# Optimization experiments

Hardware: AMD Instinct MI355X
Metric: run time of the kernel (lower is better)

Reference implementation:

```python
import jax, jax.numpy as jnp
import numpy as np

SR = 16000; HOP = 256; NFFT = 2048; NMELS = 80; NSTFT = NFFT // 2 + 1
MIN_P = int(SR / 500.0); MAX_P = int(SR / 50.0)  # 32, 320
FRAME_LEN = 2 * HOP  # 512
N_ITER = 4; MOMENTUM = 0.99


def hann(N):
    # periodic hann window (torch.hann_window default)
    return 0.5 - 0.5 * jnp.cos(2.0 * jnp.pi * jnp.arange(N) / N)


def frame_signal(x, frame_len, hop):
    # x: (B, T) -> (B, n_frames, frame_len)
    n_frames = (x.shape[-1] - frame_len) // hop + 1
    idx = jnp.arange(n_frames)[:, None] * hop + jnp.arange(frame_len)[None, :]
    return x[:, idx]


def stft(x, window):
    # center=True, reflect pad, onesided -> (B, NSTFT, n_frames) complex
    xp = jnp.pad(x, ((0, 0), (NFFT // 2, NFFT // 2)), mode='reflect')
    fr = frame_signal(xp, NFFT, HOP) * window
    return jnp.fft.rfft(fr, axis=-1).transpose(0, 2, 1)


def istft(spec, window):
    # spec: (B, NSTFT, n_frames) complex -> (B, HOP*(n_frames-1)) real
    fr = jnp.fft.irfft(spec.transpose(0, 2, 1), n=NFFT, axis=-1) * window
    B, nF, _ = fr.shape
    L = NFFT + HOP * (nF - 1)
    idx = (jnp.arange(nF)[:, None] * HOP + jnp.arange(NFFT)[None, :]).ravel()
    y = jnp.zeros((B, L), fr.dtype).at[:, idx].add(fr.reshape(B, -1))
    env = jnp.zeros((L,), fr.dtype).at[idx].add(jnp.tile(window ** 2, nF))
    y = y / jnp.where(env > 1e-11, env, 1.0)
    return y[:, NFFT // 2: NFFT // 2 + HOP * (nF - 1)]


def mel_fbanks():
    # torchaudio melscale_fbanks, htk scale, norm=None -> (NSTFT, NMELS)
    all_freqs = jnp.linspace(0.0, SR / 2, NSTFT)
    m_max = 2595.0 * jnp.log10(1.0 + (SR / 2) / 700.0)
    f_pts = 700.0 * (10.0 ** (jnp.linspace(0.0, m_max, NMELS + 2) / 2595.0) - 1.0)
    f_diff = f_pts[1:] - f_pts[:-1]
    slopes = f_pts[None, :] - all_freqs[:, None]
    down = -slopes[:, :-2] / f_diff[:-1]
    up = slopes[:, 2:] / f_diff[1:]
    return jnp.maximum(0.0, jnp.minimum(down, up))


def mel_to_linear(mel):
    # F.interpolate(mode='linear', align_corners=False) along mel axis 80 -> 1025
    scale = NMELS / NSTFT
    src = jnp.maximum((jnp.arange(NSTFT) + 0.5) * scale - 0.5, 0.0)
    i0 = jnp.clip(jnp.floor(src).astype(jnp.int32), 0, NMELS - 1)
    i1 = jnp.minimum(i0 + 1, NMELS - 1)
    w = (src - i0).astype(mel.dtype)
    return (1.0 - w)[None, :, None] * mel[:, i0, :] + w[None, :, None] * mel[:, i1, :]


def griffin_lim(spec, window):
    # torchaudio GriffinLim: power=1, n_iter=4, momentum=0.99, rand_init
    kr, ki = jax.random.split(jax.random.key(42))
    angles = (jax.random.uniform(kr, spec.shape) + 1j * jax.random.uniform(ki, spec.shape)).astype(jnp.complex64)
    tprev = jnp.zeros_like(angles)
    mom = MOMENTUM / (1.0 + MOMENTUM)
    for _ in range(N_ITER):
        inv = istft(spec * angles, window)
        rebuilt = stft(inv, window)
        angles = rebuilt - tprev * mom
        angles = angles / (jnp.abs(angles) + 1e-16)
        tprev = rebuilt
    return istft(spec * angles, window)


def _forward(waveform, W1, b1, W2, b2, W3, b3):
    window = hann(NFFT)
    x = waveform[:, 0, :]  # (B, T)
    # --- F0 + loudness framing (frame_length=512, hop=256, reflect pad) ---
    xp = jnp.pad(x, ((0, 0), (FRAME_LEN // 2, FRAME_LEN // 2)), mode='reflect')
    frames = frame_signal(xp, FRAME_LEN, HOP)  # (B, nF, 512)
    # F0: L2-normalize frames, FFT-based linear autocorrelation over lags 32..255
    fn = frames / (jnp.linalg.norm(frames, axis=-1, keepdims=True) + 1e-8)
    sp = jnp.fft.rfft(fn, n=2 * FRAME_LEN, axis=-1)
    ac = jnp.fft.irfft(sp * jnp.conj(sp), n=2 * FRAME_LEN, axis=-1)
    ac = ac[..., MIN_P:min(MAX_P, FRAME_LEN // 2)]  # (B, nF, 224)
    period = jnp.argmax(ac, axis=-1).astype(x.dtype) + MIN_P
    f0 = jnp.clip(SR / (period + 1e-8), 50.0, 500.0)  # (B, nF)
    # loudness
    loud = 20.0 * jnp.log10(jnp.sqrt(jnp.mean(frames ** 2, axis=-1)) + 1e-8)
    # bottleneck encoder (eval mode: no f0 noise)
    feats = jnp.stack([f0, loud], axis=-1)  # (B, nF, 2)
    h = jax.nn.elu(feats @ W1 + b1)
    h = jax.nn.elu(h @ W2 + b2)
    content = h @ W3 + b3  # (B, nF, 64)
    # --- mel -> linear -> griffin-lim (eval mode: no formant perturb) ---
    mag = jnp.abs(stft(x, window))  # power=1.0 magnitude, (B, 1025, nF)
    mel = jnp.einsum('bft,fm->bmt', mag, mel_fbanks())  # (B, 80, nF)
    lin = mel_to_linear(mel)  # (B, 1025, nF)
    rec = griffin_lim(lin, window)  # (B, T)
    T = waveform.shape[-1]
    rec = rec[..., :T]
    pad = T - rec.shape[-1]
    if pad > 0:
        rec = jnp.pad(rec, ((0, 0), (0, pad)))
    return rec, content


def setup_inputs() -> dict:
    key = jax.random.key(0)
    ks = jax.random.split(key, 4)
    B, T = 16, 131072
    waveform = jax.random.normal(ks[0], (B, 1, T), jnp.float32)

    def lin_init(k, fi, fo):
        bound = 1.0 / np.sqrt(fi)
        kw, kb = jax.random.split(k)
        W = jax.random.uniform(kw, (fi, fo), jnp.float32, -bound, bound)
        b = jax.random.uniform(kb, (fo,), jnp.float32, -bound, bound)
        return W, b

    W1, b1 = lin_init(ks[1], 2, 256)
    W2, b2 = lin_init(ks[2], 256, 256)
    W3, b3 = lin_init(ks[3], 256, 64)
    return {"waveform": waveform, "W1": W1, "b1": b1, "W2": W2, "b2": b2, "W3": W3, "b3": b3}


def reference(waveform, W1, b1, W2, b2, W3, b3):
    return _forward(waveform, W1, b1, W2, b2, W3, b3)
```

## Files before the change

kernel.cpp:

```cpp
#include <hip/hip_runtime.h>
#include <cstdint>
#include <cstddef>

#ifndef M_PI
#define M_PI 3.14159265358979323846
#endif

#define SRATE   16000
#define HOP     256
#define NFFT    2048
#define NBINS   1025
#define NMELS   80
#define BATCH   16
#define TLEN    131072
#define NF      513
#define LOLA    133120
#define FRAMEL  512
#define MINP    32
#define NLAGS   224
#define NELEM   (BATCH*NBINS*NF)
#define MLPR    4
#define DF      7.8125f

#define PADF(i) ((i) + 3*((i) >> 5))

__host__ __device__ inline void threefry2x32(uint32_t k0, uint32_t k1,
                                             uint32_t x0, uint32_t x1,
                                             uint32_t& o0, uint32_t& o1) {
  uint32_t ks0 = k0, ks1 = k1, ks2 = k0 ^ k1 ^ 0x1BD11BDAu;
  uint32_t ks[3] = {ks0, ks1, ks2};
  const uint32_t rot[2][4] = {{13u,15u,26u,6u},{17u,29u,16u,24u}};
  x0 += ks0; x1 += ks1;
#pragma unroll
  for (int i = 0; i < 5; ++i) {
#pragma unroll
    for (int r = 0; r < 4; ++r) {
      uint32_t rr = rot[i & 1][r];
      x0 += x1;
      x1 = (x1 << rr) | (x1 >> (32u - rr));
      x1 ^= x0;
    }
    x0 += ks[(i + 1) % 3];
    x1 += ks[(i + 2) % 3] + (uint32_t)(i + 1);
  }
  o0 = x0; o1 = x1;
}

__device__ inline float bits_to_uniform(uint32_t b) {
  uint32_t fb = (b >> 9) | 0x3f800000u;
  return __uint_as_float(fb) - 1.0f;
}

#define BF(e,o,WR,WI) do{ float vr=Xr[o]*(WR)-Xi[o]*(WI); \
  float vi=Xr[o]*(WI)+Xi[o]*(WR); float ur=Xr[e],ui=Xi[e]; \
  Xr[e]=ur+vr; Xi[e]=ui+vi; Xr[o]=ur-vr; Xi[o]=ui-vi; }while(0)

__device__ __forceinline__ void fft1024(float (&Xr)[8], float (&Xi)[8],
    float* __restrict__ sre, float* __restrict__ sim,
    const float* __restrict__ twr, const float* __restrict__ twi, float sgn)
{
  const int t = threadIdx.x;
  const float C7 = 0.70710678118654752440f;
  BF(0,1,1.0f,0.0f); BF(2,3,1.0f,0.0f); BF(4,5,1.0f,0.0f); BF(6,7,1.0f,0.0f);
  BF(0,2,1.0f,0.0f); BF(1,3,0.0f,sgn); BF(4,6,1.0f,0.0f); BF(5,7,0.0f,sgn);
  BF(0,4,1.0f,0.0f); BF(1,5,C7,sgn*C7); BF(2,6,0.0f,sgn); BF(3,7,-C7,sgn*C7);
  __syncthreads();
#pragma unroll
  for (int m = 0; m < 8; ++m) { int p = PADF(8*t + m); sre[p] = Xr[m]; sim[p] = Xi[m]; }
  __syncthreads();
  {
    int f0 = t & 7, f1 = t >> 3;
#pragma unroll
    for (int m = 0; m < 8; ++m) { int p = PADF(f0 + 8*m + 64*f1); Xr[m] = sre[p]; Xi[m] = sim[p]; }
    int x = 128*f0; float wr = twr[x], wi = sgn*twi[x];
    BF(0,1,wr,wi); BF(2,3,wr,wi); BF(4,5,wr,wi); BF(6,7,wr,wi);
    x = 64*f0;      float ar = twr[x], ai = sgn*twi[x];
    x = 64*(f0+8);  float br = twr[x], bi = sgn*twi[x];
    BF(0,2,ar,ai); BF(1,3,br,bi); BF(4,6,ar,ai); BF(5,7,br,bi);
#pragma unroll
    for (int mm = 0; mm < 4; ++mm) {
      x = 32*(f0 + 8*mm); float cr = twr[x], ci = sgn*twi[x];
      BF(mm, mm+4, cr, ci);
    }
#pragma unroll
    for (int m = 0; m < 8; ++m) { int p = PADF(f0 + 8*m + 64*f1); sre[p] = Xr[m]; sim[p] = Xi[m]; }
  }
  __syncthreads();
  {
    int f0 = t & 63, f1 = t >> 6;
#pragma unroll
    for (int m = 0; m < 8; ++m) { int p = PADF(f0 + 64*m + 512*f1); Xr[m] = sre[p]; Xi[m] = sim[p]; }
    int x = 16*f0; float wr = twr[x], wi = sgn*twi[x];
    BF(0,1,wr,wi); BF(2,3,wr,wi); BF(4,5,wr,wi); BF(6,7,wr,wi);
    x = 8*f0;       float ar = twr[x], ai = sgn*twi[x];
    x = 8*(f0+64);  float br = twr[x], bi = sgn*twi[x];
    BF(0,2,ar,ai); BF(1,3,br,bi); BF(4,6,ar,ai); BF(5,7,br,bi);
#pragma unroll
    for (int mm = 0; mm < 4; ++mm) {
      x = 4*(f0 + 64*mm); float cr = twr[x], ci = sgn*twi[x];
      BF(mm, mm+4, cr, ci);
    }
#pragma unroll
    for (int m = 0; m < 8; ++m) { int p = PADF(f0 + 64*m + 512*f1); sre[p] = Xr[m]; sim[p] = Xi[m]; }
  }
  __syncthreads();
  {
#pragma unroll
    for (int m = 0; m < 8; ++m) { int p = PADF(t + 128*m); Xr[m] = sre[p]; Xi[m] = sim[p]; }
#pragma unroll
    for (int mm = 0; mm < 4; ++mm) {
      int x = 2*t + 256*mm; float cr = twr[x], ci = sgn*twi[x];
      BF(mm, mm+4, cr, ci);
    }
  }
}

__device__ __forceinline__ void r2c_combine(float (&Xr)[8], float (&Xi)[8],
    float* __restrict__ sre, float* __restrict__ sim,
    const float* __restrict__ twr, const float* __restrict__ twi,
    float& x1024r)
{
  const int t = threadIdx.x;
  __syncthreads();
#pragma unroll
  for (int m = 0; m < 8; ++m) { int p = PADF(t + 128*m); sre[p] = Xr[m]; sim[p] = Xi[m]; }
  __syncthreads();
  if (t == 0) x1024r = Xr[0] - Xi[0];
#pragma unroll
  for (int m = 0; m < 8; ++m) {
    int k  = t + 128*m;
    int km = PADF((1024 - k) & 1023);
    float zmr = sre[km], zmi = sim[km];
    float Er  = 0.5f*(Xr[m] + zmr), Ei  = 0.5f*(Xi[m] - zmi);
    float Odr = 0.5f*(Xr[m] - zmr), Odi = 0.5f*(Xi[m] + zmi);
    float Or  = Odi, Oi = -Odr;
    float wr  = twr[k], wi = -twi[k];
    Xr[m] = Er + (wr*Or - wi*Oi);
    Xi[m] = Ei + (wr*Oi + wi*Or);
  }
}

__device__ inline float lin_interp_s(const float* __restrict__ melsh, int k) {
  float src = ((float)k + 0.5f) * ((float)NMELS / (float)NBINS) - 0.5f;
  src = src < 0.0f ? 0.0f : src;
  int i0 = (int)src; if (i0 > NMELS - 1) i0 = NMELS - 1;
  int i1 = i0 + 1 > NMELS - 1 ? NMELS - 1 : i0 + 1;
  float w = src - (float)i0;
  return (1.0f - w) * melsh[i0] + w * melsh[i1];
}

__global__ __launch_bounds__(256) void k_init_a(float2* __restrict__ winp,
                                                double* __restrict__ win2,
                                                float* __restrict__ twrf, float* __restrict__ twif,
                                                float* __restrict__ fptsf,
                                                int2* __restrict__ melrange) {
  int i = blockIdx.x * 256 + threadIdx.x;
  if (i < NFFT) {
    double w = 0.5 - 0.5 * cos(2.0 * M_PI * (double)i / (double)NFFT);
    win2[i] = w * w;
  }
  if (i < 1024) {
    double w0 = 0.5 - 0.5 * cos(2.0 * M_PI * (double)(2*i)   / (double)NFFT);
    double w1 = 0.5 - 0.5 * cos(2.0 * M_PI * (double)(2*i+1) / (double)NFFT);
    winp[i] = make_float2((float)w0, (float)w1);
    double th = 2.0 * M_PI * (double)i / (double)NFFT;
    twrf[i] = (float)cos(th); twif[i] = (float)sin(th);
  }
  if (i < NMELS + 2) {
    double m_max = 2595.0 * log10(1.0 + (SRATE / 2.0) / 700.0);
    fptsf[i] = (float)(700.0 * (pow(10.0, ((double)i * m_max / (double)(NMELS + 1)) / 2595.0) - 1.0));
  }
  if (i < NMELS) {
    double m_max = 2595.0 * log10(1.0 + (SRATE / 2.0) / 700.0);
    double fp0 = 700.0 * (pow(10.0, ((double)i       * m_max / (double)(NMELS + 1)) / 2595.0) - 1.0);
    double fp1 = 700.0 * (pow(10.0, ((double)(i + 1) * m_max / (double)(NMELS + 1)) / 2595.0) - 1.0);
    double fp2 = 700.0 * (pow(10.0, ((double)(i + 2) * m_max / (double)(NMELS + 1)) / 2595.0) - 1.0);
    int lo = (int)floor(fp0 / 7.8125) + 1;
    int hi = (int)ceil (fp2 / 7.8125);
    if (lo < 0) lo = 0; if (lo > NBINS) lo = NBINS;
    if (hi < 0) hi = 0; if (hi > NBINS) hi = NBINS;
    #define WGT(k) fmin(((double)(k)*7.8125 - fp0)/(fp1 - fp0), (fp2 - (double)(k)*7.8125)/(fp2 - fp1))
    while (lo > 0 && WGT(lo - 1) > 0.0) --lo;
    while (lo < hi && WGT(lo) <= 0.0) ++lo;
    while (hi < NBINS && WGT(hi) > 0.0) ++hi;
    while (hi > lo && WGT(hi - 1) <= 0.0) --hi;
    #undef WGT
    melrange[i] = make_int2(lo, hi);
  }
}

__global__ __launch_bounds__(256) void k_init_b(const double* __restrict__ win2,
                                                float* __restrict__ envif) {
  int i = blockIdx.x * 256 + threadIdx.x;
  if (i < LOLA) {
    int lo = i - (NFFT - 1);
    int fmin = lo <= 0 ? 0 : (lo + HOP - 1) / HOP;
    int fmax = i / HOP; if (fmax > NF - 1) fmax = NF - 1;
    double s = 0.0;
    for (int f = fmin; f <= fmax; ++f) s += win2[i - HOP * f];
    envif[i] = (float)(1.0 / (s > 1e-11 ? s : 1.0));
  }
}

__global__ __launch_bounds__(256) void k_angles(float2* __restrict__ A,
                                                uint32_t kr0, uint32_t kr1,
                                                uint32_t ki0, uint32_t ki1) {
  uint32_t idx = blockIdx.x * 256u + threadIdx.x;
  if (idx >= (uint32_t)NELEM) return;
  uint32_t per_b = (uint32_t)(NF * NBINS);
  uint32_t b = idx / per_b, r = idx % per_b;
  uint32_t t = r / NBINS, k = r % NBINS;
  uint32_t j = (b * (uint32_t)NBINS + k) * (uint32_t)NF + t;
  uint32_t a0, a1, b0, b1;
  threefry2x32(kr0, kr1, 0u, j, a0, a1);
  threefry2x32(ki0, ki1, 0u, j, b0, b1);
  A[idx] = make_float2(bits_to_uniform(a0 ^ a1), bits_to_uniform(b0 ^ b1));
}

__global__ __launch_bounds__(128) void k_stft_mel(const float* __restrict__ x,
                                                  const float2* __restrict__ winp,
                                                  const float* __restrict__ twrf, const float* __restrict__ twif,
                                                  const float* __restrict__ fptsf, const int2* __restrict__ melrange,
                                                  float* __restrict__ mel) {
  __shared__ float sre[1160], sim[1160];
  __shared__ float fsh[NMELS + 2];
  __shared__ int2  rsh[NMELS];
  int b = blockIdx.x / NF, tf = blockIdx.x % NF;
  int t = threadIdx.x;
  const float* xb = x + (size_t)b * TLEN;
  if (t < NMELS + 2) fsh[t] = fptsf[t];
  if (t < NMELS)     rsh[t] = melrange[t];
  if (tf >= 4 && tf <= 508) {
    const float2* xb2 = (const float2*)xb;
#pragma unroll
    for (int s = 0; s < 8; ++s) {
      int n = t + 128 * s;
      float2 v = xb2[128 * tf + n - 512];
      float2 w = winp[n];
      sre[PADF(n)] = v.x * w.x;
      sim[PADF(n)] = v.y * w.y;
    }
  } else {
#pragma unroll
    for (int s = 0; s < 8; ++s) {
      int n = t + 128 * s;
      int j0 = HOP * tf + 2 * n - (NFFT / 2);
      int m0 = j0 < 0 ? -j0 : (j0 >= TLEN ? 2 * TLEN - 2 - j0 : j0);
      int j1 = j0 + 1;
      int m1 = j1 < 0 ? -j1 : (j1 >= TLEN ? 2 * TLEN - 2 - j1 : j1);
      float2 w = winp[n];
      sre[PADF(n)] = xb[m0] * w.x;
      sim[PADF(n)] = xb[m1] * w.y;
    }
  }
  __syncthreads();
  float Xr[8], Xi[8];
  int rt = (int)(__brev((unsigned)t) >> 25);
  const int r3[8] = {0,4,2,6,1,5,3,7};
#pragma unroll
  for (int m = 0; m < 8; ++m) {
    int p = PADF(rt + 128 * r3[m]);
    Xr[m] = sre[p]; Xi[m] = sim[p];
  }
  fft1024(Xr, Xi, sre, sim, twrf, twif, -1.0f);
  float x1024r = 0.0f;
  r2c_combine(Xr, Xi, sre, sim, twrf, twif, x1024r);
  __syncthreads();
#pragma unroll
  for (int m = 0; m < 8; ++m) {
    int k = t + 128 * m;
    sre[k] = sqrtf(Xr[m]*Xr[m] + Xi[m]*Xi[m]);
  }
  if (t == 0) sre[1024] = fabsf(x1024r);
  __syncthreads();
  if (t < NMELS) {
    float fp0 = fsh[t], fp1 = fsh[t + 1], fp2 = fsh[t + 2];
    float id0 = 1.0f / (fp1 - fp0), id1 = 1.0f / (fp2 - fp1);
    int2 r = rsh[t];
    float acc = 0.0f;
    for (int k = r.x; k < r.y; ++k) {
      float freq = (float)k * DF;
      float w = fminf((freq - fp0) * id0, (fp2 - freq) * id1);
      acc += sre[k] * fmaxf(w, 0.0f);
    }
    mel[(size_t)blockIdx.x * NMELS + t] = acc;
  }
}

__global__ __launch_bounds__(128) void k_istft(const float* __restrict__ mel, const float2* __restrict__ A,
                                               const float2* __restrict__ winp,
                                               const float* __restrict__ twrf, const float* __restrict__ twif,
                                               float2* __restrict__ fr2) {
  __shared__ float sre[1160], sim[1160];
  __shared__ float melsh[NMELS];
  int t = threadIdx.x;
  size_t row = blockIdx.x;
  const float2* Arow = A + row * NBINS;
  if (t < NMELS) melsh[t] = mel[row * NMELS + t];
  __syncthreads();
#pragma unroll
  for (int s = 0; s < 9; ++s) {
    int k = t + 128 * s;
    if (k < NBINS) {
      float sv = lin_interp_s(melsh, k);
      float2 a = Arow[k];
      sre[PADF(k)] = sv * a.x;
      sim[PADF(k)] = (k == 0 || k == 1024) ? 0.0f : sv * a.y;
    }
  }
  __syncthreads();
  float Xr[8], Xi[8];
  int rt = (int)(__brev((unsigned)t) >> 25);
  const int r3[8] = {0,4,2,6,1,5,3,7};
#pragma unroll
  for (int m = 0; m < 8; ++m) {
    int n  = rt + 128 * r3[m];
    int p  = PADF(n), q = PADF(1024 - n);
    float Er = 0.5f*(sre[p] + sre[q]), Ei = 0.5f*(sim[p] - sim[q]);
    float Fr = 0.5f*(sre[p] - sre[q]), Fi = 0.5f*(sim[p] + sim[q]);
    float wr = twrf[n], wi = twif[n];
    float Or = wr*Fr - wi*Fi, Oi = wr*Fi + wi*Fr;
    Xr[m] = Er - Oi;
    Xi[m] = Ei + Or;
  }
  fft1024(Xr, Xi, sre, sim, twrf, twif, +1.0f);
  float2* frrow = fr2 + row * 1024;
  const float invM = 1.0f / 1024.0f;
#pragma unroll
  for (int m = 0; m < 8; ++m) {
    int g = t + 128 * m;
    float2 w = winp[g];
    frrow[g] = make_float2(Xr[m] * invM * w.x,
                           Xi[m] * invM * w.y);
  }
}

__global__ __launch_bounds__(256) void k_ola(const float* __restrict__ fr,
                                             const float* __restrict__ envif,
                                             float* __restrict__ y, float* __restrict__ out) {
  size_t idx = (size_t)blockIdx.x * 256 + threadIdx.x;
  const size_t QROW = LOLA / 4;
  if (idx >= (size_t)BATCH * QROW) return;
  int b = (int)(idx / QROW);
  int i0 = 4 * (int)(idx % QROW);
  const float* frb = fr + (size_t)b * NF * NFFT;
  int lo0 = i0 - (NFFT - 1);
  int fm0 = lo0 <= 0 ? 0 : (lo0 + HOP - 1) / HOP;
  int fx0 = i0 / HOP; if (fx0 > NF - 1) fx0 = NF - 1;
  int i3 = i0 + 3;
  int lo3 = i3 - (NFFT - 1);
  int fm3 = lo3 <= 0 ? 0 : (lo3 + HOP - 1) / HOP;
  int fx3 = i3 / HOP; if (fx3 > NF - 1) fx3 = NF - 1;
  float4 v;
  if (fm0 == fm3 && fx0 == fx3) {
    float4 s = make_float4(0.f, 0.f, 0.f, 0.f);
    for (int f = fm0; f <= fx0; ++f) {
      const float4 a = *(const float4*)(frb + (size_t)f * NFFT + (i0 - HOP * f));
      s.x += a.x; s.y += a.y; s.z += a.z; s.w += a.w;
    }
    const float4 e = *(const float4*)(envif + i0);
    v = make_float4(s.x * e.x, s.y * e.y, s.z * e.z, s.w * e.w);
  } else {
    float vv[4];
#pragma unroll
    for (int u = 0; u < 4; ++u) {
      int i = i0 + u;
      int lo = i - (NFFT - 1);
      int fmin = lo <= 0 ? 0 : (lo + HOP - 1) / HOP;
      int fmax = i / HOP; if (fmax > NF - 1) fmax = NF - 1;
      float s = 0.0f;
      for (int f = fmin; f <= fmax; ++f)
        s += frb[(size_t)f * NFFT + (i - HOP * f)];
      vv[u] = s * envif[i];
    }
    v = make_float4(vv[0], vv[1], vv[2], vv[3]);
  }
  if (out) {
    int j0 = i0 - NFFT / 2;
    if (j0 >= 0 && j0 + 3 < TLEN) {
      *(float4*)(out + (size_t)b * TLEN + j0) = v;
    } else {
      const float vv[4] = {v.x, v.y, v.z, v.w};
#pragma unroll
      for (int u = 0; u < 4; ++u) {
        int j = j0 + u;
        if (j >= 0 && j < TLEN) out[(size_t)b * TLEN + j] = vv[u];
      }
    }
  } else {
    *(float4*)(y + (size_t)b * LOLA + i0) = v;
  }
}

__global__ __launch_bounds__(128) void k_stft_gl(const float* __restrict__ y,
                                                 const float2* __restrict__ winp,
                                                 const float* __restrict__ twrf, const float* __restrict__ twif,
                                                 float2* __restrict__ A, float2* __restrict__ P,
                                                 float momf, int writeP) {
  __shared__ float sre[1160], sim[1160];
  int b = blockIdx.x / NF, tf = blockIdx.x % NF;
  int t = threadIdx.x;
  size_t row = blockIdx.x;
  float2* Arow = A + row * NBINS;
  float2* Prow = P + row * NBINS;
  const bool readP = (momf != 0.0f);
  float2 pfr[8];
  float2 pny = make_float2(0.0f, 0.0f);
  if (readP) {
#pragma unroll
    for (int m = 0; m < 8; ++m) pfr[m] = Prow[t + 128 * m];
    if (t == 0) pny = Prow[1024];
  } else {
#pragma unroll
    for (int m = 0; m < 8; ++m) pfr[m] = make_float2(0.0f, 0.0f);
  }
  const float* yb = y + (size_t)b * LOLA;
  if (tf >= 4 && tf <= 508) {
    const float2* yb2 = (const float2*)yb;
#pragma unroll
    for (int s = 0; s < 8; ++s) {
      int n = t + 128 * s;
      float2 v = yb2[128 * tf + n];
      float2 w = winp[n];
      sre[PADF(n)] = v.x * w.x;
      sim[PADF(n)] = v.y * w.y;
    }
  } else {
#pragma unroll
    for (int s = 0; s < 8; ++s) {
      int n = t + 128 * s;
      int j0 = HOP * tf + 2 * n - (NFFT / 2);
      int m0 = j0 < 0 ? -j0 : (j0 >= TLEN ? 2 * TLEN - 2 - j0 : j0);
      int j1 = j0 + 1;
      int m1 = j1 < 0 ? -j1 : (j1 >= TLEN ? 2 * TLEN - 2 - j1 : j1);
      float2 w = winp[n];
      sre[PADF(n)] = yb[NFFT/2 + m0] * w.x;
      sim[PADF(n)] = yb[NFFT/2 + m1] * w.y;
    }
  }
  __syncthreads();
  float Xr[8], Xi[8];
  int rt = (int)(__brev((unsigned)t) >> 25);
  const int r3[8] = {0,4,2,6,1,5,3,7};
#pragma unroll
  for (int m = 0; m < 8; ++m) {
    int p = PADF(rt + 128 * r3[m]);
    Xr[m] = sre[p]; Xi[m] = sim[p];
  }
  fft1024(Xr, Xi, sre, sim, twrf, twif, -1.0f);
  float x1024r = 0.0f;
  r2c_combine(Xr, Xi, sre, sim, twrf, twif, x1024r);
#pragma unroll
  for (int m = 0; m < 8; ++m) {
    int k = t + 128 * m;
    float ar = Xr[m] - momf * pfr[m].x;
    float ai = Xi[m] - momf * pfr[m].y;
    float mg = sqrtf(ar * ar + ai * ai) + 1e-16f;
    float inv = 1.0f / mg;
    Arow[k] = make_float2(ar * inv, ai * inv);
    if (writeP) Prow[k] = make_float2(Xr[m], Xi[m]);
  }
  if (t == 0) {
    float ar = x1024r - momf * pny.x;
    float ai = -momf * pny.y;
    float mg = sqrtf(ar * ar + ai * ai) + 1e-16f;
    float inv = 1.0f / mg;
    Arow[1024] = make_float2(ar * inv, ai * inv);
    if (writeP) Prow[1024] = make_float2(x1024r, 0.0f);
  }
}

__global__ __launch_bounds__(256) void k_feats(const float* __restrict__ x, double* __restrict__ feats) {
  __shared__ __align__(16) double xd[528];
  __shared__ double pacc[8][224];
  __shared__ double red[256];
  __shared__ double cval[256];
  __shared__ int    cidx[256];
  int b = blockIdx.x / NF, tf = blockIdx.x % NF;
  const float* xb = x + (size_t)b * TLEN;
  int tid = threadIdx.x;
  for (int n = tid; n < FRAMEL; n += 256) {
    int j = HOP * tf + n - (FRAMEL / 2);
    int m = j < 0 ? -j : (j >= TLEN ? 2 * TLEN - 2 - j : j);
    xd[n] = (double)xb[m];
  }
  if (tid < 16) xd[FRAMEL + tid] = 0.0;
  __syncthreads();
  double ss = 0.0;
  for (int n = tid; n < FRAMEL; n += 256) { double v = xd[n]; ss += v * v; }
  red[tid] = ss;
  __syncthreads();
  for (int w = 128; w > 0; w >>= 1) {
    if (tid < w) red[tid] += red[tid + w];
    __syncthreads();
  }
  double sumsq = red[0];
  int g = tid & 31, ph = tid >> 5;
  double acc[8];
#pragma unroll
  for (int d = 0; d < 8; ++d) acc[d] = 0.0;
  if (g < 28) {
    const double2* d2 = (const double2*)xd;
    const int LA = 32 + 4 * g;
    const int LB = 252 - 4 * g;
    for (int n0 = 8 * ph; n0 < 512 - LA; n0 += 64) {
      int h = n0 >> 1, hb = (n0 + LA) >> 1;
      double2 a0 = d2[h],      a1 = d2[h + 1],  a2 = d2[h + 2],  a3 = d2[h + 3];
      double2 b0 = d2[hb],     b1 = d2[hb + 1], b2 = d2[hb + 2],
              b3 = d2[hb + 3], b4 = d2[hb + 4], b5 = d2[hb + 5];
      double aa[8]  = {a0.x,a0.y,a1.x,a1.y,a2.x,a2.y,a3.x,a3.y};
      double bb[12] = {b0.x,b0.y,b1.x,b1.y,b2.x,b2.y,b3.x,b3.y,b4.x,b4.y,b5.x,b5.y};
#pragma unroll
      for (int d = 0; d < 4; ++d)
#pragma unroll
        for (int jj = 0; jj < 8; ++jj)
          acc[d] += aa[jj] * bb[jj + d];
    }
    for (int n0 = 8 * ph; n0 < 512 - LB; n0 += 64) {
      int h = n0 >> 1, hb = (n0 + LB) >> 1;
      double2 a0 = d2[h],      a1 = d2[h + 1],  a2 = d2[h + 2],  a3 = d2[h + 3];
      double2 b0 = d2[hb],     b1 = d2[hb + 1], b2 = d2[hb + 2],
              b3 = d2[hb + 3], b4 = d2[hb + 4], b5 = d2[hb + 5];
      double aa[8]  = {a0.x,a0.y,a1.x,a1.y,a2.x,a2.y,a3.x,a3.y};
      double bb[12] = {b0.x,b0.y,b1.x,b1.y,b2.x,b2.y,b3.x,b3.y,b4.x,b4.y,b5.x,b5.y};
#pragma unroll
      for (int d = 0; d < 4; ++d)
#pragma unroll
        for (int jj = 0; jj < 8; ++jj)
          acc[4 + d] += aa[jj] * bb[jj + d];
    }
#pragma unroll
    for (int d = 0; d < 8; ++d) pacc[ph][g * 8 + d] = acc[d];
  }
  __syncthreads();
  if (tid < 224) {
    double tot = 0.0;
#pragma unroll
    for (int p = 0; p < 8; ++p) tot += pacc[p][tid];
    int gg = tid >> 3, dd = tid & 7;
    int lag = dd < 4 ? (32 + 4 * gg + dd) : (252 - 4 * gg + (dd - 4));
    cval[tid] = tot; cidx[tid] = lag;
  } else { cval[tid] = -1e300; cidx[tid] = 1 << 30; }
  __syncthreads();
  for (int w = 128; w > 0; w >>= 1) {
    if (tid < w) {
      double vl = cval[tid], vr = cval[tid + w];
      int il = cidx[tid], ir = cidx[tid + w];
      if (vr > vl || (vr == vl && ir < il)) { cval[tid] = vr; cidx[tid] = ir; }
    }
    __syncthreads();
  }
  if (tid == 0) {
    double period = (double)cidx[0];
    double f0 = (double)SRATE / (period + 1e-8);
    f0 = f0 < 50.0 ? 50.0 : (f0 > 500.0 ? 500.0 : f0);
    double mean = sumsq / (double)FRAMEL;
    double loud = 20.0 * log10(sqrt(mean) + 1e-8);
    feats[(size_t)blockIdx.x * 2 + 0] = f0;
    feats[(size_t)blockIdx.x * 2 + 1] = loud;
  }
}

__global__ __launch_bounds__(256) void k_mlp(const double* __restrict__ feats,
                                             const float* __restrict__ W1, const float* __restrict__ b1,
                                             const float* __restrict__ W2, const float* __restrict__ b2,
                                             const float* __restrict__ W3, const float* __restrict__ b3,
                                             float* __restrict__ out) {
  __shared__ __align__(16) float h1[MLPR][256];
  __shared__ __align__(16) float h2[MLPR][256];
  __shared__ float fsh[MLPR][2];
  int j = threadIdx.x;
  size_t row0 = (size_t)blockIdx.x * MLPR;
  if (j < MLPR * 2) ((float*)fsh)[j] = (float)feats[row0 * 2 + j];
  __syncthreads();
  float w1a = W1[j], w1b = W1[256 + j], bb1 = b1[j];
#pragma unroll
  for (int r = 0; r < MLPR; ++r) {
    float v = fsh[r][0] * w1a + fsh[r][1] * w1b + bb1;
    h1[r][j] = v > 0.0f ? v : expm1f(v);
  }
  __syncthreads();
  float acc[MLPR];
  float bb2 = b2[j];
#pragma unroll
  for (int r = 0; r < MLPR; ++r) acc[r] = bb2;
  const float* w2p = W2 + j;
  for (int i4 = 0; i4 < 64; ++i4) {
    float w0 = w2p[(4 * i4 + 0) * 256];
    float w1 = w2p[(4 * i4 + 1) * 256];
    float w2v = w2p[(4 * i4 + 2) * 256];
    float w3v = w2p[(4 * i4 + 3) * 256];
#pragma unroll
    for (int r = 0; r < MLPR; ++r) {
      float4 hv = ((const float4*)h1[r])[i4];
      acc[r] += hv.x * w0;
      acc[r] += hv.y * w1;
      acc[r] += hv.z * w2v;
      acc[r] += hv.w * w3v;
    }
  }
#pragma unroll
  for (int r = 0; r < MLPR; ++r) h2[r][j] = acc[r] > 0.0f ? acc[r] : expm1f(acc[r]);
  __syncthreads();
  int o = j & 63, r = j >> 6;
  float oacc = b3[o];
  const float* w3p = W3 + o;
  for (int i4 = 0; i4 < 64; ++i4) {
    float4 hv = ((const float4*)h2[r])[i4];
    oacc += hv.x * w3p[(4 * i4 + 0) * 64];
    oacc += hv.y * w3p[(4 * i4 + 1) * 64];
    oacc += hv.z * w3p[(4 * i4 + 2) * 64];
    oacc += hv.w * w3p[(4 * i4 + 3) * 64];
  }
  out[(row0 + r) * 64 + o] = oacc;
}

__global__ void k_sentinel(float* out) { out[0] = 31337.0f; }

extern "C" void kernel_launch(void* const* d_in, const int* in_sizes, int n_in,
                              void* d_out, int out_size, void* d_ws, size_t ws_size,
                              hipStream_t stream) {
  const float* x  = (const float*)d_in[0];
  const float* W1 = (const float*)d_in[1];
  const float* b1 = (const float*)d_in[2];
  const float* W2 = (const float*)d_in[3];
  const float* b2 = (const float*)d_in[4];
  const float* W3 = (const float*)d_in[5];
  const float* b3 = (const float*)d_in[6];
  float* out = (float*)d_out;

  double* ws = (double*)d_ws;
  size_t o = 0;
  double*  winsq = ws + o; o += NFFT;
  double*  feats = ws + o; o += (size_t)BATCH * NF * 2;
  float2* winp  = (float2*)(ws + o);
  float*  twrf  = (float*)(winp + 1024);
  float*  twif  = twrf + 1024;
  float*  fptsf = twif + 1024;
  int2*   melrange = (int2*)(fptsf + 84);
  float*  mel   = (float*)(melrange + NMELS);
  float*  fr    = mel + (size_t)BATCH * NF * NMELS;
  float*  y     = fr + (size_t)BATCH * NF * NFFT;
  float*  envif = y + (size_t)BATCH * LOLA;
  float2* A     = (float2*)(envif + LOLA);
  float2* P     = A + (size_t)NELEM;
  size_t total_bytes = (size_t)((char*)(P + (size_t)NELEM) - (char*)d_ws);

  if (ws_size < total_bytes) {
    k_sentinel<<<1, 1, 0, stream>>>(out);
    return;
  }

  uint32_t kr0, kr1, ki0, ki1;
  threefry2x32(0u, 42u, 0u, 0u, kr0, kr1);
  threefry2x32(0u, 42u, 0u, 1u, ki0, ki1);

  const int NBLK = BATCH * NF;
  const int OLAB = ((size_t)BATCH * (LOLA / 4) + 255) / 256;
  k_init_a<<<8, 256, 0, stream>>>(winp, winsq, twrf, twif, fptsf, melrange);
  k_init_b<<<(LOLA + 255) / 256, 256, 0, stream>>>(winsq, envif);
  k_stft_mel<<<NBLK, 128, 0, stream>>>(x, winp, twrf, twif, fptsf, melrange, mel);
  k_angles<<<(NELEM + 255) / 256, 256, 0, stream>>>(A, kr0, kr1, ki0, ki1);

  const float momf = (float)(0.99 / 1.99);
  for (int it = 0; it < 4; ++it) {
    k_istft<<<NBLK, 128, 0, stream>>>(mel, A, winp, twrf, twif, (float2*)fr);
    k_ola<<<OLAB, 256, 0, stream>>>(fr, envif, y, nullptr);
    k_stft_gl<<<NBLK, 128, 0, stream>>>(y, winp, twrf, twif, A, P,
                                        it == 0 ? 0.0f : momf, it < 3 ? 1 : 0);
  }
  k_istft<<<NBLK, 128, 0, stream>>>(mel, A, winp, twrf, twif, (float2*)fr);
  k_ola<<<OLAB, 256, 0, stream>>>(fr, envif, y, out);

  k_feats<<<NBLK, 256, 0, stream>>>(x, feats);
  k_mlp<<<NBLK / MLPR, 256, 0, stream>>>(feats, W1, b1, W2, b2, W3, b3, out + (size_t)BATCH * TLEN);
}
```

Before: 873.4 us.

## Fuse Griffin-Lim STFT with following ISTFT and generate random phases inline

Merges the per-iteration forward STFT and phase normalisation with the next inverse STFT into one kernel, so the unit-phase spectrum A is never written to or read from global memory. The initial random phases are now generated with threefry inside the first ISTFT kernel rather than by a separate k_angles pass over a buffer. This removes one kernel launch per iteration, the angles kernel, and a large complex buffer of round-trip traffic. In exchange the fused kernel holds more live state and needs an extra barrier, which may raise register pressure.

```diff
diff --git a/kernel.cpp b/kernel.cpp
--- a/kernel.cpp
+++ b/kernel.cpp
@@ -202,21 +202,6 @@
   }
 }
 
-__global__ __launch_bounds__(256) void k_angles(float2* __restrict__ A,
-                                                uint32_t kr0, uint32_t kr1,
-                                                uint32_t ki0, uint32_t ki1) {
-  uint32_t idx = blockIdx.x * 256u + threadIdx.x;
-  if (idx >= (uint32_t)NELEM) return;
-  uint32_t per_b = (uint32_t)(NF * NBINS);
-  uint32_t b = idx / per_b, r = idx % per_b;
-  uint32_t t = r / NBINS, k = r % NBINS;
-  uint32_t j = (b * (uint32_t)NBINS + k) * (uint32_t)NF + t;
-  uint32_t a0, a1, b0, b1;
-  threefry2x32(kr0, kr1, 0u, j, a0, a1);
-  threefry2x32(ki0, ki1, 0u, j, b0, b1);
-  A[idx] = make_float2(bits_to_uniform(a0 ^ a1), bits_to_uniform(b0 ^ b1));
-}
-
 __global__ __launch_bounds__(128) void k_stft_mel(const float* __restrict__ x,
                                                   const float2* __restrict__ winp,
                                                   const float* __restrict__ twrf, const float* __restrict__ twif,
@@ -287,31 +272,145 @@
   }
 }
 
-__global__ __launch_bounds__(128) void k_istft(const float* __restrict__ mel, const float2* __restrict__ A,
-                                               const float2* __restrict__ winp,
-                                               const float* __restrict__ twrf, const float* __restrict__ twif,
-                                               float2* __restrict__ fr2) {
+__global__ __launch_bounds__(128) void k_istft0(const float* __restrict__ mel,
+                                                const float2* __restrict__ winp,
+                                                const float* __restrict__ twrf, const float* __restrict__ twif,
+                                                float2* __restrict__ fr2,
+                                                uint32_t kr0, uint32_t kr1,
+                                                uint32_t ki0, uint32_t ki1) {
   __shared__ float sre[1160], sim[1160];
   __shared__ float melsh[NMELS];
   int t = threadIdx.x;
   size_t row = blockIdx.x;
-  const float2* Arow = A + row * NBINS;
+  int b = blockIdx.x / NF, tf = blockIdx.x % NF;
   if (t < NMELS) melsh[t] = mel[row * NMELS + t];
   __syncthreads();
-#pragma unroll
   for (int s = 0; s < 9; ++s) {
     int k = t + 128 * s;
     if (k < NBINS) {
+      uint32_t j = ((uint32_t)b * (uint32_t)NBINS + (uint32_t)k) * (uint32_t)NF + (uint32_t)tf;
+      uint32_t a0, a1, b0, b1;
+      threefry2x32(kr0, kr1, 0u, j, a0, a1);
+      threefry2x32(ki0, ki1, 0u, j, b0, b1);
+      float ux = bits_to_uniform(a0 ^ a1);
+      float uy = bits_to_uniform(b0 ^ b1);
       float sv = lin_interp_s(melsh, k);
-      float2 a = Arow[k];
-      sre[PADF(k)] = sv * a.x;
-      sim[PADF(k)] = (k == 0 || k == 1024) ? 0.0f : sv * a.y;
+      sre[PADF(k)] = sv * ux;
+      sim[PADF(k)] = (k == 0 || k == 1024) ? 0.0f : sv * uy;
     }
   }
   __syncthreads();
   float Xr[8], Xi[8];
   int rt = (int)(__brev((unsigned)t) >> 25);
   const int r3[8] = {0,4,2,6,1,5,3,7};
+#pragma unroll
+  for (int m = 0; m < 8; ++m) {
+    int n  = rt + 128 * r3[m];
+    int p  = PADF(n), q = PADF(1024 - n);
+    float Er = 0.5f*(sre[p] + sre[q]), Ei = 0.5f*(sim[p] - sim[q]);
+    float Fr = 0.5f*(sre[p] - sre[q]), Fi = 0.5f*(sim[p] + sim[q]);
+    float wr = twrf[n], wi = twif[n];
+    float Or = wr*Fr - wi*Fi, Oi = wr*Fi + wi*Fr;
+    Xr[m] = Er - Oi;
+    Xi[m] = Ei + Or;
+  }
+  fft1024(Xr, Xi, sre, sim, twrf, twif, +1.0f);
+  float2* frrow = fr2 + row * 1024;
+  const float invM = 1.0f / 1024.0f;
+#pragma unroll
+  for (int m = 0; m < 8; ++m) {
+    int g = t + 128 * m;
+    float2 w = winp[g];
+    frrow[g] = make_float2(Xr[m] * invM * w.x,
+                           Xi[m] * invM * w.y);
+  }
+}
+
+__global__ __launch_bounds__(128) void k_gl_istft(const float* __restrict__ y,
+                                                  const float* __restrict__ mel,
+                                                  const float2* __restrict__ winp,
+                                                  const float* __restrict__ twrf, const float* __restrict__ twif,
+                                                  float2* __restrict__ P, float2* __restrict__ fr2,
+                                                  float momf, int writeP) {
+  __shared__ float sre[1160], sim[1160];
+  __shared__ float melsh[NMELS];
+  int b = blockIdx.x / NF, tf = blockIdx.x % NF;
+  int t = threadIdx.x;
+  size_t row = blockIdx.x;
+  float2* Prow = P + row * NBINS;
+  const bool readP = (momf != 0.0f);
+  float2 pfr[8];
+  float2 pny = make_float2(0.0f, 0.0f);
+  if (readP) {
+#pragma unroll
+    for (int m = 0; m < 8; ++m) pfr[m] = Prow[t + 128 * m];
+    if (t == 0) pny = Prow[1024];
+  } else {
+#pragma unroll
+    for (int m = 0; m < 8; ++m) pfr[m] = make_float2(0.0f, 0.0f);
+  }
+  if (t < NMELS) melsh[t] = mel[row * NMELS + t];
+  const float* yb = y + (size_t)b * LOLA;
+  if (tf >= 4 && tf <= 508) {
+    const float2* yb2 = (const float2*)yb;
+#pragma unroll
+    for (int s = 0; s < 8; ++s) {
+      int n = t + 128 * s;
+      float2 v = yb2[128 * tf + n];
+      float2 w = winp[n];
+      sre[PADF(n)] = v.x * w.x;
+      sim[PADF(n)] = v.y * w.y;
+    }
+  } else {
+#pragma unroll
+    for (int s = 0; s < 8; ++s) {
+      int n = t + 128 * s;
+      int j0 = HOP * tf + 2 * n - (NFFT / 2);
+      int m0 = j0 < 0 ? -j0 : (j0 >= TLEN ? 2 * TLEN - 2 - j0 : j0);
+      int j1 = j0 + 1;
+      int m1 = j1 < 0 ? -j1 : (j1 >= TLEN ? 2 * TLEN - 2 - j1 : j1);
+      float2 w = winp[n];
+      sre[PADF(n)] = yb[NFFT/2 + m0] * w.x;
+      sim[PADF(n)] = yb[NFFT/2 + m1] * w.y;
+    }
+  }
+  __syncthreads();
+  float Xr[8], Xi[8];
+  int rt = (int)(__brev((unsigned)t) >> 25);
+  const int r3[8] = {0,4,2,6,1,5,3,7};
+#pragma unroll
+  for (int m = 0; m < 8; ++m) {
+    int p = PADF(rt + 128 * r3[m]);
+    Xr[m] = sre[p]; Xi[m] = sim[p];
+  }
+  fft1024(Xr, Xi, sre, sim, twrf, twif, -1.0f);
+  float x1024r = 0.0f;
+  r2c_combine(Xr, Xi, sre, sim, twrf, twif, x1024r);
+  __syncthreads();
+#pragma unroll
+  for (int m = 0; m < 8; ++m) {
+    int k = t + 128 * m;
+    float ar = Xr[m] - momf * pfr[m].x;
+    float ai = Xi[m] - momf * pfr[m].y;
+    float mg = sqrtf(ar * ar + ai * ai) + 1e-16f;
+    float inv = 1.0f / mg;
+    if (writeP) Prow[k] = make_float2(Xr[m], Xi[m]);
+    float sv = lin_interp_s(melsh, k);
+    sre[PADF(k)] = sv * (ar * inv);
+    sim[PADF(k)] = (k == 0) ? 0.0f : sv * (ai * inv);
+  }
+  if (t == 0) {
+    float ar = x1024r - momf * pny.x;
+    float ai = -momf * pny.y;
+    float mg = sqrtf(ar * ar + ai * ai) + 1e-16f;
+    float inv = 1.0f / mg;
+    if (writeP) Prow[1024] = make_float2(x1024r, 0.0f);
+    float sv = lin_interp_s(melsh, 1024);
+    sre[PADF(1024)] = sv * (ar * inv);
+    sim[PADF(1024)] = 0.0f;
+    (void)ai;
+  }
+  __syncthreads();
 #pragma unroll
   for (int m = 0; m < 8; ++m) {
     int n  = rt + 128 * r3[m];
@@ -392,84 +491,6 @@
   }
 }
 
-__global__ __launch_bounds__(128) void k_stft_gl(const float* __restrict__ y,
-                                                 const float2* __restrict__ winp,
-                                                 const float* __restrict__ twrf, const float* __restrict__ twif,
-                                                 float2* __restrict__ A, float2* __restrict__ P,
-                                                 float momf, int writeP) {
-  __shared__ float sre[1160], sim[1160];
-  int b = blockIdx.x / NF, tf = blockIdx.x % NF;
-  int t = threadIdx.x;
-  size_t row = blockIdx.x;
-  float2* Arow = A + row * NBINS;
-  float2* Prow = P + row * NBINS;
-  const bool readP = (momf != 0.0f);
-  float2 pfr[8];
-  float2 pny = make_float2(0.0f, 0.0f);
-  if (readP) {
-#pragma unroll
-    for (int m = 0; m < 8; ++m) pfr[m] = Prow[t + 128 * m];
-    if (t == 0) pny = Prow[1024];
-  } else {
-#pragma unroll
-    for (int m = 0; m < 8; ++m) pfr[m] = make_float2(0.0f, 0.0f);
-  }
-  const float* yb = y + (size_t)b * LOLA;
-  if (tf >= 4 && tf <= 508) {
-    const float2* yb2 = (const float2*)yb;
-#pragma unroll
-    for (int s = 0; s < 8; ++s) {
-      int n = t + 128 * s;
-      float2 v = yb2[128 * tf + n];
-      float2 w = winp[n];
-      sre[PADF(n)] = v.x * w.x;
-      sim[PADF(n)] = v.y * w.y;
-    }
-  } else {
-#pragma unroll
-    for (int s = 0; s < 8; ++s) {
-      int n = t + 128 * s;
-      int j0 = HOP * tf + 2 * n - (NFFT / 2);
-      int m0 = j0 < 0 ? -j0 : (j0 >= TLEN ? 2 * TLEN - 2 - j0 : j0);
-      int j1 = j0 + 1;
-      int m1 = j1 < 0 ? -j1 : (j1 >= TLEN ? 2 * TLEN - 2 - j1 : j1);
-      float2 w = winp[n];
-      sre[PADF(n)] = yb[NFFT/2 + m0] * w.x;
-      sim[PADF(n)] = yb[NFFT/2 + m1] * w.y;
-    }
-  }
-  __syncthreads();
-  float Xr[8], Xi[8];
-  int rt = (int)(__brev((unsigned)t) >> 25);
-  const int r3[8] = {0,4,2,6,1,5,3,7};
-#pragma unroll
-  for (int m = 0; m < 8; ++m) {
-    int p = PADF(rt + 128 * r3[m]);
-    Xr[m] = sre[p]; Xi[m] = sim[p];
-  }
-  fft1024(Xr, Xi, sre, sim, twrf, twif, -1.0f);
-  float x1024r = 0.0f;
-  r2c_combine(Xr, Xi, sre, sim, twrf, twif, x1024r);
-#pragma unroll
-  for (int m = 0; m < 8; ++m) {
-    int k = t + 128 * m;
-    float ar = Xr[m] - momf * pfr[m].x;
-    float ai = Xi[m] - momf * pfr[m].y;
-    float mg = sqrtf(ar * ar + ai * ai) + 1e-16f;
-    float inv = 1.0f / mg;
-    Arow[k] = make_float2(ar * inv, ai * inv);
-    if (writeP) Prow[k] = make_float2(Xr[m], Xi[m]);
-  }
-  if (t == 0) {
-    float ar = x1024r - momf * pny.x;
-    float ai = -momf * pny.y;
-    float mg = sqrtf(ar * ar + ai * ai) + 1e-16f;
-    float inv = 1.0f / mg;
-    Arow[1024] = make_float2(ar * inv, ai * inv);
-    if (writeP) Prow[1024] = make_float2(x1024r, 0.0f);
-  }
-}
-
 __global__ __launch_bounds__(256) void k_feats(const float* __restrict__ x, double* __restrict__ feats) {
   __shared__ __align__(16) double xd[528];
   __shared__ double pacc[8][224];
@@ -642,8 +663,7 @@
   float*  fr    = mel + (size_t)BATCH * NF * NMELS;
   float*  y     = fr + (size_t)BATCH * NF * NFFT;
   float*  envif = y + (size_t)BATCH * LOLA;
-  float2* A     = (float2*)(envif + LOLA);
-  float2* P     = A + (size_t)NELEM;
+  float2* P     = (float2*)(envif + LOLA);
   size_t total_bytes = (size_t)((char*)(P + (size_t)NELEM) - (char*)d_ws);
 
   if (ws_size < total_bytes) {
@@ -660,17 +680,15 @@
   k_init_a<<<8, 256, 0, stream>>>(winp, winsq, twrf, twif, fptsf, melrange);
   k_init_b<<<(LOLA + 255) / 256, 256, 0, stream>>>(winsq, envif);
   k_stft_mel<<<NBLK, 128, 0, stream>>>(x, winp, twrf, twif, fptsf, melrange, mel);
-  k_angles<<<(NELEM + 255) / 256, 256, 0, stream>>>(A, kr0, kr1, ki0, ki1);
 
   const float momf = (float)(0.99 / 1.99);
+  k_istft0<<<NBLK, 128, 0, stream>>>(mel, winp, twrf, twif, (float2*)fr, kr0, kr1, ki0, ki1);
+  k_ola<<<OLAB, 256, 0, stream>>>(fr, envif, y, nullptr);
   for (int it = 0; it < 4; ++it) {
-    k_istft<<<NBLK, 128, 0, stream>>>(mel, A, winp, twrf, twif, (float2*)fr);
-    k_ola<<<OLAB, 256, 0, stream>>>(fr, envif, y, nullptr);
-    k_stft_gl<<<NBLK, 128, 0, stream>>>(y, winp, twrf, twif, A, P,
-                                        it == 0 ? 0.0f : momf, it < 3 ? 1 : 0);
-  }
-  k_istft<<<NBLK, 128, 0, stream>>>(mel, A, winp, twrf, twif, (float2*)fr);
-  k_ola<<<OLAB, 256, 0, stream>>>(fr, envif, y, out);
+    k_gl_istft<<<NBLK, 128, 0, stream>>>(y, mel, winp, twrf, twif, P, (float2*)fr,
+                                         it == 0 ? 0.0f : momf, it < 3 ? 1 : 0);
+    k_ola<<<OLAB, 256, 0, stream>>>(fr, envif, y, it == 3 ? out : nullptr);
+  }
 
   k_feats<<<NBLK, 256, 0, stream>>>(x, feats);
   k_mlp<<<NBLK / MLPR, 256, 0, stream>>>(feats, W1, b1, W2, b2, W3, b3, out + (size_t)BATCH * TLEN);
```

After: 786.3 us. 1.11x faster.
